# Performance work log

Measured on AMD Instinct MI355X. Metric: run time of the kernel, lower is better.

Reference implementation:

```python
import jax, jax.numpy as jnp
import numpy as np

BS = 1
H_ = 200
W_ = 200
NQ = H_ * W_          # 40000 BEV queries == num_value
D = 256
NH = 8
DH = D // NH          # 32
NL = 1
NP = 4
NQUEUE = 2
B2 = BS * NQUEUE


def setup_inputs() -> dict:
    key = jax.random.key(0)
    ks = jax.random.split(key, 12)
    s = 0.02
    inp = {
        "query": jax.random.normal(ks[0], (BS, NQ, D), jnp.float32),
        "query_pos": jax.random.normal(ks[1], (BS, NQ, D), jnp.float32) * 0.1,
        "reference_points": jax.random.uniform(ks[2], (BS, NQ, NL, 2), jnp.float32),
        # sampling_offsets linear: in = d_model*num_bev_queue, out = queue*heads*levels*points*2
        "W_so": jax.random.normal(ks[3], (D * NQUEUE, NQUEUE * NH * NL * NP * 2), jnp.float32) * s,
        "b_so": jax.random.normal(ks[4], (NQUEUE * NH * NL * NP * 2,), jnp.float32),
        # attention_weights linear: out = queue*heads*levels*points
        "W_aw": jax.random.normal(ks[5], (D * NQUEUE, NQUEUE * NH * NL * NP), jnp.float32) * s,
        "b_aw": jax.random.normal(ks[6], (NQUEUE * NH * NL * NP,), jnp.float32) * s,
        "W_v": jax.random.normal(ks[7], (D, D), jnp.float32) * s,
        "b_v": jax.random.normal(ks[8], (D,), jnp.float32) * s,
        "W_o": jax.random.normal(ks[9], (D, D), jnp.float32) * s,
        "b_o": jax.random.normal(ks[10], (D,), jnp.float32) * s,
    }
    return inp


def _deform_attn_single_level(v, loc, attn_w):
    """v: (B, Nv, NH, DH); loc: (B, Nq, NH, NP, 2) in [0,1]; attn_w: (B, Nq, NH, NP).
    grid_sample semantics: align_corners=False, zero padding."""
    B = v.shape[0]
    vt = v.transpose(0, 2, 1, 3)                      # (B, NH, Nv, DH)
    # pixel coords (align_corners=False): p = loc * size - 0.5
    x = (loc[..., 0] * W_ - 0.5).transpose(0, 2, 1, 3).reshape(B, NH, -1)  # (B, NH, Nq*NP)
    y = (loc[..., 1] * H_ - 0.5).transpose(0, 2, 1, 3).reshape(B, NH, -1)
    wt = attn_w.transpose(0, 2, 1, 3).reshape(B, NH, -1)
    x0f = jnp.floor(x); y0f = jnp.floor(y)
    x0 = x0f.astype(jnp.int32); y0 = y0f.astype(jnp.int32)
    x1 = x0 + 1; y1 = y0 + 1
    wx1 = x - x0f; wx0 = 1.0 - wx1
    wy1 = y - y0f; wy0 = 1.0 - wy1

    def corner(ix, iy, cw):
        valid = (ix >= 0) & (ix < W_) & (iy >= 0) & (iy < H_)
        idx = jnp.clip(iy, 0, H_ - 1) * W_ + jnp.clip(ix, 0, W_ - 1)
        g = jnp.take_along_axis(vt, idx[..., None], axis=2)   # (B, NH, Nq*NP, DH)
        return g * (cw * valid.astype(cw.dtype))[..., None]

    acc = (corner(x0, y0, wx0 * wy0) + corner(x1, y0, wx1 * wy0)
           + corner(x0, y1, wx0 * wy1) + corner(x1, y1, wx1 * wy1))
    acc = acc * wt[..., None]
    acc = acc.reshape(B, NH, -1, NP, DH).sum(3)               # (B, NH, Nq, DH)
    return acc.transpose(0, 2, 1, 3).reshape(B, -1, NH * DH)  # (B, Nq, D)


def reference(query, query_pos, reference_points, W_so, b_so, W_aw, b_aw, W_v, b_v, W_o, b_o):
    # input_flatten defaults to query (pre-positional); query gets pos added
    q = query + query_pos
    # default queue construction: duplicate current BEV -> (bs*queue, Nv, D)
    value = jnp.stack([query, query], axis=1).reshape(B2, NQ, D)
    history_bev = value[:BS]                                   # (bs, Nv, D)
    qwh = jnp.concatenate([history_bev, q], axis=-1)           # (bs, Nq, 2D)
    # value projection
    v = (value @ W_v + b_v).reshape(B2, NQ, NH, DH)
    # offsets / weights from concatenated features
    so = (qwh @ W_so + b_so).reshape(BS, NQ, NH, NQUEUE, NL, NP, 2)
    aw = (qwh @ W_aw + b_aw).reshape(BS, NQ, NH, NQUEUE, NL * NP)
    aw = jax.nn.softmax(aw, axis=-1).reshape(BS, NQ, NH, NQUEUE, NL, NP)
    aw = aw.transpose(0, 3, 1, 2, 4, 5).reshape(B2, NQ, NH, NL, NP)
    so = so.transpose(0, 3, 1, 2, 4, 5, 6).reshape(B2, NQ, NH, NL, NP, 2)
    # duplicate reference points across the queue
    rp = jnp.stack([reference_points] * NQUEUE, axis=1).reshape(B2, NQ, NL, 2)
    offset_norm = jnp.array([W_, H_], jnp.float32)             # (w, h)
    loc = rp[:, :, None, :, None, :] + so / offset_norm        # (B2, NQ, NH, NL, NP, 2)
    out = _deform_attn_single_level(v, loc[:, :, :, 0], aw[:, :, :, 0])  # (B2, NQ, D)
    # fuse queue outputs by mean (queue is the fast axis of B2)
    out = out.reshape(BS, NQUEUE, NQ, D).mean(axis=1)
    return out @ W_o + b_o
```

## Files before the change

kernel.cpp:

```cpp
#include <hip/hip_runtime.h>
#include <math.h>

#define NQc 40000
#define Wc 200
#define Hc 200

typedef __attribute__((ext_vector_type(8))) short short8;
typedef __attribute__((ext_vector_type(4))) float f32x4;
typedef __attribute__((ext_vector_type(2))) float f32x2;

#define VMWAIT(N) asm volatile("s_waitcnt vmcnt(" #N ")" ::: "memory")

__device__ __forceinline__ ushort f2b(float f) {
  unsigned u = __float_as_uint(f);
  u = (u + 0x7fffu + ((u >> 16) & 1u)) >> 16;
  return (ushort)u;
}

__device__ __forceinline__ void glds16(const void* g, void* l) {
  __builtin_amdgcn_global_load_lds(
      (const __attribute__((address_space(1))) void*)g,
      (__attribute__((address_space(3))) void*)l, 16, 0, 0);
}

__global__ __launch_bounds__(256) void prep_all(
    const float* __restrict__ q, const float* __restrict__ qp,
    const float* __restrict__ Wv, const float* __restrict__ Wo,
    const float* __restrict__ Wso, const float* __restrict__ Waw,
    ushort* __restrict__ qlo, ushort* __restrict__ qhi,
    ushort* __restrict__ WvT, ushort* __restrict__ WoT,
    ushort* __restrict__ WsoT, ushort* __restrict__ WawT) {
  const int bid = blockIdx.x;
  if (bid < 10000) {
    const int flat = bid * 256 + threadIdx.x;
    const int m = flat >> 6;
    const int c8 = (flat & 63) * 8;
    ushort o[8];
    if (c8 < 256) {
      const float4 a = *(const float4*)(q + (size_t)m * 256 + c8);
      const float4 b = *(const float4*)(q + (size_t)m * 256 + c8 + 4);
      o[0] = f2b(a.x); o[1] = f2b(a.y); o[2] = f2b(a.z); o[3] = f2b(a.w);
      o[4] = f2b(b.x); o[5] = f2b(b.y); o[6] = f2b(b.z); o[7] = f2b(b.w);
      *(uint4*)&qlo[(size_t)m * 256 + c8] = *(const uint4*)o;
    } else {
      const int c = c8 - 256;
      const float4 a  = *(const float4*)(q  + (size_t)m * 256 + c);
      const float4 b  = *(const float4*)(q  + (size_t)m * 256 + c + 4);
      const float4 ap = *(const float4*)(qp + (size_t)m * 256 + c);
      const float4 bp = *(const float4*)(qp + (size_t)m * 256 + c + 4);
      o[0] = f2b(a.x + ap.x); o[1] = f2b(a.y + ap.y);
      o[2] = f2b(a.z + ap.z); o[3] = f2b(a.w + ap.w);
      o[4] = f2b(b.x + bp.x); o[5] = f2b(b.y + bp.y);
      o[6] = f2b(b.z + bp.z); o[7] = f2b(b.w + bp.w);
      *(uint4*)&qhi[(size_t)m * 256 + c] = *(const uint4*)o;
    }
  } else {
    const int idx = (bid - 10000) * 256 + threadIdx.x;
    if (idx < 65536) {
      int n = idx >> 8, k = idx & 255;
      WvT[idx] = f2b(Wv[k * 256 + n]);
    } else if (idx < 131072) {
      int i = idx - 65536;
      int n = i >> 8, k = i & 255;
      WoT[i] = f2b(Wo[k * 256 + n]);
    } else if (idx < 196608) {
      int i = idx - 131072;
      int n = i >> 9, k = i & 511;
      WsoT[i] = f2b(Wso[k * 128 + n]);
    } else {
      int i = idx - 196608;
      int n = i >> 9, k = i & 511;
      WawT[i] = f2b(Waw[k * 64 + n]);
    }
  }
}


__global__ __launch_bounds__(256, 2) void gemm_soaw_k(
    const ushort* __restrict__ qlo, const ushort* __restrict__ qhi,
    const ushort* __restrict__ WsoT, const ushort* __restrict__ WawT,
    const float* __restrict__ b_so, const float* __restrict__ b_aw,
    float* __restrict__ so_ws, float* __restrict__ aw_ws) {
  __shared__ __align__(16) char smem[65536];
  float (*E)[68] = (float(*)[68])smem;
  f32x4 acc[12] = {};
  const int m0 = blockIdx.x * 64;
  const int tid = threadIdx.x;
  const int w = tid >> 6, lane = tid & 63;
  const int rl = lane & 15, q2 = lane >> 4;
  const int sw8 = rl & 7;
  const int lrow = lane >> 3, lch = (lane & 7) ^ (lrow & 7);

  auto STAGE = [&](int buf, int t) {
    ushort* As = (ushort*)(smem + buf * 32768);
    ushort* Bs = As + 4096;
    const int k0 = t * 64;
    const ushort* aq = (k0 < 256) ? qlo : qhi;
    const int ka = k0 & 255;
#pragma unroll
    for (int i = 0; i < 2; ++i) {
      const int g = w * 2 + i;
      const int row = g * 8 + lrow;
      glds16(aq + (size_t)(m0 + row) * 256 + ka + lch * 8,
             As + g * 512 + lane * 8);
    }
#pragma unroll
    for (int i = 0; i < 6; ++i) {
      const int g = w * 6 + i;
      const int row = g * 8 + lrow;
      const ushort* gsrc = (row < 128)
          ? WsoT + (size_t)row * 512 + k0 + lch * 8
          : WawT + (size_t)(row - 128) * 512 + k0 + lch * 8;
      glds16(gsrc, Bs + g * 512 + lane * 8);
    }
  };

  STAGE(0, 0);
#pragma unroll
  for (int t = 0; t < 8; ++t) {
    const int cur = t & 1;
    if (t < 7) {
      STAGE(cur ^ 1, t + 1);
      VMWAIT(8);
    } else {
      VMWAIT(0);
    }
    __builtin_amdgcn_s_barrier();
    {
      const ushort* Asb = (const ushort*)(smem + cur * 32768);
      const ushort* Bsb = Asb + 4096;
#pragma unroll
      for (int kk = 0; kk < 2; ++kk) {
        const short8 af = *(const short8*)
            &Asb[(w * 16 + rl) * 64 + ((kk * 4 + q2) ^ sw8) * 8];
#pragma unroll
        for (int nj = 0; nj < 12; ++nj) {
          const short8 bf = *(const short8*)
              &Bsb[(nj * 16 + rl) * 64 + ((kk * 4 + q2) ^ sw8) * 8];
          acc[nj] = __builtin_amdgcn_mfma_f32_16x16x32_bf16(af, bf, acc[nj], 0, 0, 0);
        }
      }
    }
    __builtin_amdgcn_s_barrier();
  }

  const int rbase = q2 * 4, cl = rl;
#pragma unroll
  for (int p = 0; p < 3; ++p) {
#pragma unroll
    for (int j = 0; j < 4; ++j) {
      const int nj = p * 4 + j;
      const int nl = j * 16 + cl;
      const f32x4 a = acc[nj];
      if (p < 2) {
        const float bb = b_so[p * 64 + nl];
#pragma unroll
        for (int r = 0; r < 4; ++r)
          E[w * 16 + rbase + r][nl] = a[r] + bb;
      } else {
        const float bb = b_aw[nl];
#pragma unroll
        for (int r = 0; r < 4; ++r) {
          float z = a[r] + bb;
          float zm = fmaxf(z, __shfl_xor(z, 1, 64));
          zm = fmaxf(zm, __shfl_xor(zm, 2, 64));
          float e = expf(z - zm);
          float s = e + __shfl_xor(e, 1, 64);
          s = s + __shfl_xor(s, 2, 64);
          E[w * 16 + rbase + r][nl] = e / s;
        }
      }
    }
    __syncthreads();
#pragma unroll
    for (int it = 0; it < 4; ++it) {
      const int flat = it * 256 + tid;
      const int row = flat >> 4, c4 = (flat & 15) * 4;
      const float4 vle = *(const float4*)&E[row][c4];
      if (p < 2)
        *(float4*)&so_ws[(size_t)(m0 + row) * 128 + p * 64 + c4] = vle;
      else
        *(float4*)&aw_ws[(size_t)(m0 + row) * 64 + c4] = vle;
    }
    __syncthreads();
  }
}

__global__ __launch_bounds__(256, 3) void gemm_v_k(
    const ushort* __restrict__ qlo, const ushort* __restrict__ WvT,
    const float* __restrict__ bv, ushort* __restrict__ vt) {
  __shared__ __align__(16) char smem[49152];
  ushort (*Eb)[72] = (ushort(*)[72])smem;
  f32x4 acc[8] = {};
  const int m0 = blockIdx.x * 64, n0 = blockIdx.y * 128;
  const int tid = threadIdx.x;
  const int w = tid >> 6, lane = tid & 63;
  const int rl = lane & 15, q2 = lane >> 4;
  const int sw8 = rl & 7;
  const int lrow = lane >> 3, lch = (lane & 7) ^ (lrow & 7);

  auto STAGE = [&](int buf, int t) {
    ushort* As = (ushort*)(smem + buf * 24576);
    ushort* Bs = As + 4096;
    const int k0 = t * 64;
#pragma unroll
    for (int i = 0; i < 2; ++i) {
      const int g = w * 2 + i;
      const int row = g * 8 + lrow;
      glds16(qlo + (size_t)(m0 + row) * 256 + k0 + lch * 8,
             As + g * 512 + lane * 8);
    }
#pragma unroll
    for (int i = 0; i < 4; ++i) {
      const int g = w * 4 + i;
      const int row = g * 8 + lrow;
      glds16(WvT + (size_t)(n0 + row) * 256 + k0 + lch * 8,
             Bs + g * 512 + lane * 8);
    }
  };

  STAGE(0, 0);
#pragma unroll
  for (int t = 0; t < 4; ++t) {
    const int cur = t & 1;
    if (t < 3) {
      STAGE(cur ^ 1, t + 1);
      VMWAIT(6);
    } else {
      VMWAIT(0);
    }
    __builtin_amdgcn_s_barrier();
    {
      const ushort* Asb = (const ushort*)(smem + cur * 24576);
      const ushort* Bsb = Asb + 4096;
#pragma unroll
      for (int kk = 0; kk < 2; ++kk) {
        const short8 af = *(const short8*)
            &Asb[(w * 16 + rl) * 64 + ((kk * 4 + q2) ^ sw8) * 8];
#pragma unroll
        for (int nj = 0; nj < 8; ++nj) {
          const short8 bf = *(const short8*)
              &Bsb[(nj * 16 + rl) * 64 + ((kk * 4 + q2) ^ sw8) * 8];
          acc[nj] = __builtin_amdgcn_mfma_f32_16x16x32_bf16(af, bf, acc[nj], 0, 0, 0);
        }
      }
    }
    __builtin_amdgcn_s_barrier();
  }

  const int rbase = q2 * 4, cl = rl;
#pragma unroll
  for (int p = 0; p < 2; ++p) {
#pragma unroll
    for (int j = 0; j < 4; ++j) {
      const int nj = p * 4 + j;
      const int n = n0 + p * 64 + j * 16 + cl;
      const float bb = bv[n];
      const f32x4 a = acc[nj];
#pragma unroll
      for (int r = 0; r < 4; ++r)
        Eb[w * 16 + rbase + r][j * 16 + cl] = f2b(a[r] + bb);
    }
    __syncthreads();
#pragma unroll
    for (int hh = 0; hh < 2; ++hh) {
      const int h = (n0 + p * 64) / 32 + hh;
#pragma unroll
      for (int it = 0; it < 2; ++it) {
        const int flat = it * 256 + tid;
        const int row = flat >> 3, d4 = (flat & 7) * 4;
        *(ushort4*)&vt[((size_t)h * NQc + m0 + row) * 32 + d4] =
            *(const ushort4*)&Eb[row][hh * 32 + d4];
      }
    }
    __syncthreads();
  }
}

__global__ __launch_bounds__(256, 3) void gemm_o_k(
    const ushort* __restrict__ Ap, const ushort* __restrict__ WoT,
    const float* __restrict__ bo, float* __restrict__ out) {
  __shared__ __align__(16) char smem[49152];
  float (*E)[68] = (float(*)[68])smem;
  f32x4 acc[8] = {};
  const int m0 = blockIdx.x * 64, n0 = blockIdx.y * 128;
  const int tid = threadIdx.x;
  const int w = tid >> 6, lane = tid & 63;
  const int rl = lane & 15, q2 = lane >> 4;
  const int sw8 = rl & 7;
  const int lrow = lane >> 3, lch = (lane & 7) ^ (lrow & 7);

  auto STAGE = [&](int buf, int t) {
    ushort* As = (ushort*)(smem + buf * 24576);
    ushort* Bs = As + 4096;
    const int k0 = t * 64;
#pragma unroll
    for (int i = 0; i < 2; ++i) {
      const int g = w * 2 + i;
      const int row = g * 8 + lrow;
      glds16(Ap + (size_t)(m0 + row) * 256 + k0 + lch * 8,
             As + g * 512 + lane * 8);
    }
#pragma unroll
    for (int i = 0; i < 4; ++i) {
      const int g = w * 4 + i;
      const int row = g * 8 + lrow;
      glds16(WoT + (size_t)(n0 + row) * 256 + k0 + lch * 8,
             Bs + g * 512 + lane * 8);
    }
  };

  STAGE(0, 0);
#pragma unroll
  for (int t = 0; t < 4; ++t) {
    const int cur = t & 1;
    if (t < 3) {
      STAGE(cur ^ 1, t + 1);
      VMWAIT(6);
    } else {
      VMWAIT(0);
    }
    __builtin_amdgcn_s_barrier();
    {
      const ushort* Asb = (const ushort*)(smem + cur * 24576);
      const ushort* Bsb = Asb + 4096;
#pragma unroll
      for (int kk = 0; kk < 2; ++kk) {
        const short8 af = *(const short8*)
            &Asb[(w * 16 + rl) * 64 + ((kk * 4 + q2) ^ sw8) * 8];
#pragma unroll
        for (int nj = 0; nj < 8; ++nj) {
          const short8 bf = *(const short8*)
              &Bsb[(nj * 16 + rl) * 64 + ((kk * 4 + q2) ^ sw8) * 8];
          acc[nj] = __builtin_amdgcn_mfma_f32_16x16x32_bf16(af, bf, acc[nj], 0, 0, 0);
        }
      }
    }
    __builtin_amdgcn_s_barrier();
  }

  const int rbase = q2 * 4, cl = rl;
#pragma unroll
  for (int p = 0; p < 2; ++p) {
#pragma unroll
    for (int j = 0; j < 4; ++j) {
      const int nj = p * 4 + j;
      const int n = n0 + p * 64 + j * 16 + cl;
      const float bb = bo[n];
      const f32x4 a = acc[nj];
#pragma unroll
      for (int r = 0; r < 4; ++r)
        E[w * 16 + rbase + r][j * 16 + cl] = a[r] + bb;
    }
    __syncthreads();
#pragma unroll
    for (int it = 0; it < 4; ++it) {
      const int flat = it * 256 + tid;
      const int row = flat >> 4, c4 = (flat & 15) * 4;
      *(float4*)&out[(size_t)(m0 + row) * 256 + n0 + p * 64 + c4] =
          *(const float4*)&E[row][c4];
    }
    __syncthreads();
  }
}

__global__ __launch_bounds__(256) void sample_kernel(
    const ushort* __restrict__ vt,
    const float* __restrict__ so_ws,
    const float* __restrict__ aw_ws,
    const float* __restrict__ refp,
    ushort* __restrict__ out_pre)
{
  __shared__ int2   offs[32][9];
  __shared__ float2 wts2[32][9][2];
  const int h  = blockIdx.x & 7;
  const int m0 = (blockIdx.x >> 3) * 32;
  const int tid = threadIdx.x;

  {
    const int j  = tid & 7;
    const int qi = tid >> 3;
    const int m  = m0 + qi;
    const int c  = h * 8 + j;
    const float sx  = so_ws[(size_t)m * 128 + c * 2 + 0];
    const float sy  = so_ws[(size_t)m * 128 + c * 2 + 1];
    const float wgt = 0.5f * aw_ws[(size_t)m * 64 + c];
    const float x = refp[m * 2 + 0] * (float)Wc + sx - 0.5f;
    const float y = refp[m * 2 + 1] * (float)Hc + sy - 0.5f;
    const float x0f = floorf(x), y0f = floorf(y);
    const int x0 = (int)x0f, y0 = (int)y0f;
    const int x1 = x0 + 1, y1 = y0 + 1;
    const float wx1 = x - x0f, wx0 = 1.0f - wx1;
    const float wy1 = y - y0f, wy0 = 1.0f - wy1;
    const float wx0v = (x0 >= 0 && x0 < Wc) ? wx0 : 0.0f;
    const float wx1v = (x1 >= 0 && x1 < Wc) ? wx1 : 0.0f;
    const float wy0v = ((y0 >= 0 && y0 < Hc) ? wy0 : 0.0f) * wgt;
    const float wy1v = ((y1 >= 0 && y1 < Hc) ? wy1 : 0.0f) * wgt;
    const int bx = min(max(x0, 0), Wc - 2);
    const float wl = (bx == x0) ? wx0v : ((bx == x1) ? wx1v : 0.0f);
    const float wr = (bx + 1 == x1) ? wx1v : ((bx + 1 == x0) ? wx0v : 0.0f);
    const int cy0 = min(max(y0, 0), Hc - 1);
    const int cy1 = min(max(y1, 0), Hc - 1);
    offs[qi][j] = make_int2((cy0 * Wc + bx) * 64, (cy1 * Wc + bx) * 64);
    wts2[qi][j][0] = make_float2(wl * wy0v, wl * wy1v);
    wts2[qi][j][1] = make_float2(wr * wy0v, wr * wy1v);
  }
  __syncthreads();

  const int qi = tid >> 3;
  const int ld = tid & 7;
  const int m  = m0 + qi;
  const int hf = ld >> 2;
  const char* __restrict__ vb =
      (const char*)(vt + (size_t)h * NQc * 32) + (uint)(ld * 16);

  uint4 raw[16];
#pragma unroll
  for (int j = 0; j < 8; ++j) {
    const int2 oo = offs[qi][j];
    raw[2 * j]     = *(const uint4*)(vb + (uint)oo.x);
    raw[2 * j + 1] = *(const uint4*)(vb + (uint)oo.y);
  }
  __builtin_amdgcn_sched_barrier(0);

  f32x2 acc0 = {0.0f, 0.0f}, acc1 = {0.0f, 0.0f};
  f32x2 acc2 = {0.0f, 0.0f}, acc3 = {0.0f, 0.0f};

#pragma unroll
  for (int j = 0; j < 8; ++j) {
    const float2 wp = wts2[qi][j][hf];
#pragma unroll
    for (int r = 0; r < 2; ++r) {
      const uint4 rawv = raw[2 * j + r];
      const float w = (r == 0) ? wp.x : wp.y;
      const f32x2 wv = {w, w};
      f32x2 v0, v1, v2, v3;
      v0.x = __uint_as_float(rawv.x << 16);
      v0.y = __uint_as_float(rawv.x & 0xFFFF0000u);
      v1.x = __uint_as_float(rawv.y << 16);
      v1.y = __uint_as_float(rawv.y & 0xFFFF0000u);
      v2.x = __uint_as_float(rawv.z << 16);
      v2.y = __uint_as_float(rawv.z & 0xFFFF0000u);
      v3.x = __uint_as_float(rawv.w << 16);
      v3.y = __uint_as_float(rawv.w & 0xFFFF0000u);
#if __has_builtin(__builtin_elementwise_fma)
      acc0 = __builtin_elementwise_fma(wv, v0, acc0);
      acc1 = __builtin_elementwise_fma(wv, v1, acc1);
      acc2 = __builtin_elementwise_fma(wv, v2, acc2);
      acc3 = __builtin_elementwise_fma(wv, v3, acc3);
#else
      acc0.x = fmaf(w, v0.x, acc0.x); acc0.y = fmaf(w, v0.y, acc0.y);
      acc1.x = fmaf(w, v1.x, acc1.x); acc1.y = fmaf(w, v1.y, acc1.y);
      acc2.x = fmaf(w, v2.x, acc2.x); acc2.y = fmaf(w, v2.y, acc2.y);
      acc3.x = fmaf(w, v3.x, acc3.x); acc3.y = fmaf(w, v3.y, acc3.y);
#endif
    }
  }

  float a[8] = {acc0.x, acc0.y, acc1.x, acc1.y,
                acc2.x, acc2.y, acc3.x, acc3.y};
#pragma unroll
  for (int k = 0; k < 8; ++k) a[k] += __shfl_xor(a[k], 4, 64);

  if (hf == 0) {
    ushort rr[8];
#pragma unroll
    for (int k = 0; k < 8; ++k) rr[k] = f2b(a[k]);
    *(uint4*)&out_pre[(size_t)m * 256 + h * 32 + ld * 8] = *(const uint4*)rr;
  }
}

extern "C" void kernel_launch(void* const* d_in, const int* in_sizes, int n_in,
                              void* d_out, int out_size, void* d_ws, size_t ws_size,
                              hipStream_t stream) {
  const float* query     = (const float*)d_in[0];
  const float* query_pos = (const float*)d_in[1];
  const float* refp      = (const float*)d_in[2];
  const float* W_so      = (const float*)d_in[3];
  const float* b_so      = (const float*)d_in[4];
  const float* W_aw      = (const float*)d_in[5];
  const float* b_aw      = (const float*)d_in[6];
  const float* W_v       = (const float*)d_in[7];
  const float* b_v       = (const float*)d_in[8];
  const float* W_o       = (const float*)d_in[9];
  const float* b_o       = (const float*)d_in[10];
  float* out = (float*)d_out;

  char* base = (char*)d_ws;
  ushort* qlo     = (ushort*)base;
  ushort* qhi     = (ushort*)(base + 20480000);
  ushort* vt      = (ushort*)(base + 20480000);
  ushort* out_pre = (ushort*)base;
  float*  so_ws   = (float*)(base + 40960000);
  float*  aw_ws   = (float*)(base + 61440000);
  ushort* WvT     = (ushort*)(base + 71680000);
  ushort* WoT     = WvT + 65536;
  ushort* WsoT    = WoT + 65536;
  ushort* WawT    = WsoT + 65536;

  prep_all<<<10896, 256, 0, stream>>>(query, query_pos, W_v, W_o, W_so, W_aw,
                                      qlo, qhi, WvT, WoT, WsoT, WawT);
  gemm_soaw_k<<<625, 256, 0, stream>>>(qlo, qhi, WsoT, WawT,
                                       b_so, b_aw, so_ws, aw_ws);
  gemm_v_k<<<dim3(625, 2), 256, 0, stream>>>(qlo, WvT, b_v, vt);
  sample_kernel<<<10000, 256, 0, stream>>>(vt, so_ws, aw_ws, refp, out_pre);
  gemm_o_k<<<dim3(625, 2), 256, 0, stream>>>(out_pre, WoT, b_o, out);
}
```

Baseline: 226.6 us.

## Fuse query bf16 conversion, value GEMM and offset/weight GEMM into one kernel

The query and query_pos conversion to bf16 now happens directly into shared memory inside a single fused front kernel. That kernel computes both the value projection and the sampling-offset/attention-weight projection from the same resident A tile, so the qlo/qhi intermediates are no longer written to and read back from global memory, and two launches are removed. In exchange it uses 128KB of LDS and large accumulator register sets, which limits occupancy to one block per CU with only 625 blocks.

Measured after the change: 237.6 us. 4.9% more time.

```diff
diff --git a/kernel.cpp b/kernel.cpp
--- a/kernel.cpp
+++ b/kernel.cpp
@@ -23,67 +23,44 @@
       (__attribute__((address_space(3))) void*)l, 16, 0, 0);
 }
 
-__global__ __launch_bounds__(256) void prep_all(
-    const float* __restrict__ q, const float* __restrict__ qp,
+__global__ __launch_bounds__(256) void prep_w(
     const float* __restrict__ Wv, const float* __restrict__ Wo,
     const float* __restrict__ Wso, const float* __restrict__ Waw,
-    ushort* __restrict__ qlo, ushort* __restrict__ qhi,
     ushort* __restrict__ WvT, ushort* __restrict__ WoT,
     ushort* __restrict__ WsoT, ushort* __restrict__ WawT) {
-  const int bid = blockIdx.x;
-  if (bid < 10000) {
-    const int flat = bid * 256 + threadIdx.x;
-    const int m = flat >> 6;
-    const int c8 = (flat & 63) * 8;
-    ushort o[8];
-    if (c8 < 256) {
-      const float4 a = *(const float4*)(q + (size_t)m * 256 + c8);
-      const float4 b = *(const float4*)(q + (size_t)m * 256 + c8 + 4);
-      o[0] = f2b(a.x); o[1] = f2b(a.y); o[2] = f2b(a.z); o[3] = f2b(a.w);
-      o[4] = f2b(b.x); o[5] = f2b(b.y); o[6] = f2b(b.z); o[7] = f2b(b.w);
-      *(uint4*)&qlo[(size_t)m * 256 + c8] = *(const uint4*)o;
-    } else {
-      const int c = c8 - 256;
-      const float4 a  = *(const float4*)(q  + (size_t)m * 256 + c);
-      const float4 b  = *(const float4*)(q  + (size_t)m * 256 + c + 4);
-      const float4 ap = *(const float4*)(qp + (size_t)m * 256 + c);
-      const float4 bp = *(const float4*)(qp + (size_t)m * 256 + c + 4);
-      o[0] = f2b(a.x + ap.x); o[1] = f2b(a.y + ap.y);
-      o[2] = f2b(a.z + ap.z); o[3] = f2b(a.w + ap.w);
-      o[4] = f2b(b.x + bp.x); o[5] = f2b(b.y + bp.y);
-      o[6] = f2b(b.z + bp.z); o[7] = f2b(b.w + bp.w);
-      *(uint4*)&qhi[(size_t)m * 256 + c] = *(const uint4*)o;
-    }
+  const int idx = blockIdx.x * 256 + threadIdx.x;
+  if (idx < 65536) {
+    int n = idx >> 8, k = idx & 255;
+    WvT[idx] = f2b(Wv[k * 256 + n]);
+  } else if (idx < 131072) {
+    int i = idx - 65536;
+    int n = i >> 8, k = i & 255;
+    WoT[i] = f2b(Wo[k * 256 + n]);
+  } else if (idx < 196608) {
+    int i = idx - 131072;
+    int n = i >> 9, k = i & 511;
+    WsoT[i] = f2b(Wso[k * 128 + n]);
   } else {
-    const int idx = (bid - 10000) * 256 + threadIdx.x;
-    if (idx < 65536) {
-      int n = idx >> 8, k = idx & 255;
-      WvT[idx] = f2b(Wv[k * 256 + n]);
-    } else if (idx < 131072) {
-      int i = idx - 65536;
-      int n = i >> 8, k = i & 255;
-      WoT[i] = f2b(Wo[k * 256 + n]);
-    } else if (idx < 196608) {
-      int i = idx - 131072;
-      int n = i >> 9, k = i & 511;
-      WsoT[i] = f2b(Wso[k * 128 + n]);
-    } else {
-      int i = idx - 196608;
-      int n = i >> 9, k = i & 511;
-      WawT[i] = f2b(Waw[k * 64 + n]);
-    }
-  }
-}
-
-
-__global__ __launch_bounds__(256, 2) void gemm_soaw_k(
-    const ushort* __restrict__ qlo, const ushort* __restrict__ qhi,
-    const ushort* __restrict__ WsoT, const ushort* __restrict__ WawT,
-    const float* __restrict__ b_so, const float* __restrict__ b_aw,
-    float* __restrict__ so_ws, float* __restrict__ aw_ws) {
-  __shared__ __align__(16) char smem[65536];
-  float (*E)[68] = (float(*)[68])smem;
-  f32x4 acc[12] = {};
+    int i = idx - 196608;
+    int n = i >> 9, k = i & 511;
+    WawT[i] = f2b(Waw[k * 64 + n]);
+  }
+}
+
+__global__ __launch_bounds__(256, 1) void fused_front(
+    const float* __restrict__ q, const float* __restrict__ qp,
+    const ushort* __restrict__ WvT, const ushort* __restrict__ WsoT,
+    const ushort* __restrict__ WawT,
+    const float* __restrict__ bv, const float* __restrict__ b_so,
+    const float* __restrict__ b_aw,
+    ushort* __restrict__ vt, float* __restrict__ so_ws,
+    float* __restrict__ aw_ws) {
+  __shared__ __align__(16) char smem[131072];
+  ushort* Ab = (ushort*)smem;
+  float (*E)[68] = (float(*)[68])(smem + 65536);
+  ushort (*Eb)[72] = (ushort(*)[72])(smem + 65536);
+  f32x4 vacc[16] = {};
+  f32x4 sacc[12] = {};
   const int m0 = blockIdx.x * 64;
   const int tid = threadIdx.x;
   const int w = tid >> 6, lane = tid & 63;
@@ -91,53 +68,94 @@
   const int sw8 = rl & 7;
   const int lrow = lane >> 3, lch = (lane & 7) ^ (lrow & 7);
 
-  auto STAGE = [&](int buf, int t) {
-    ushort* As = (ushort*)(smem + buf * 32768);
-    ushort* Bs = As + 4096;
+  {
+    const int arow = tid >> 2, qn = tid & 3;
+    const float* qr  = q  + (size_t)(m0 + arow) * 256 + qn * 64;
+    const float* qpr = qp + (size_t)(m0 + arow) * 256 + qn * 64;
+    ushort* Alo = Ab + arow * 256;
+    ushort* Ahi = Ab + 16384 + arow * 256;
+    const int swz = arow & 7;
+#pragma unroll
+    for (int i = 0; i < 4; ++i) {
+      float4 a[4], p[4];
+#pragma unroll
+      for (int k = 0; k < 4; ++k) a[k] = *(const float4*)(qr + i * 16 + k * 4);
+#pragma unroll
+      for (int k = 0; k < 4; ++k) p[k] = *(const float4*)(qpr + i * 16 + k * 4);
+      ushort lo[16], hi[16];
+#pragma unroll
+      for (int k = 0; k < 4; ++k) {
+        lo[k * 4 + 0] = f2b(a[k].x); lo[k * 4 + 1] = f2b(a[k].y);
+        lo[k * 4 + 2] = f2b(a[k].z); lo[k * 4 + 3] = f2b(a[k].w);
+        hi[k * 4 + 0] = f2b(a[k].x + p[k].x); hi[k * 4 + 1] = f2b(a[k].y + p[k].y);
+        hi[k * 4 + 2] = f2b(a[k].z + p[k].z); hi[k * 4 + 3] = f2b(a[k].w + p[k].w);
+      }
+      const int cb = qn * 8 + i * 2;
+      *(uint4*)&Alo[(cb ^ swz) * 8]       = *(const uint4*)&lo[0];
+      *(uint4*)&Alo[((cb + 1) ^ swz) * 8] = *(const uint4*)&lo[8];
+      *(uint4*)&Ahi[(cb ^ swz) * 8]       = *(const uint4*)&hi[0];
+      *(uint4*)&Ahi[((cb + 1) ^ swz) * 8] = *(const uint4*)&hi[8];
+    }
+  }
+  __syncthreads();
+
+  auto STAGEV = [&](int buf, int t) {
+    ushort* Bs = (ushort*)(smem + 65536 + buf * 32768);
     const int k0 = t * 64;
-    const ushort* aq = (k0 < 256) ? qlo : qhi;
-    const int ka = k0 & 255;
-#pragma unroll
-    for (int i = 0; i < 2; ++i) {
-      const int g = w * 2 + i;
+#pragma unroll
+    for (int i = 0; i < 8; ++i) {
+      const int g = w * 8 + i;
       const int row = g * 8 + lrow;
-      glds16(aq + (size_t)(m0 + row) * 256 + ka + lch * 8,
-             As + g * 512 + lane * 8);
-    }
+      glds16(WvT + (size_t)row * 256 + k0 + lch * 8, Bs + g * 512 + lane * 8);
+    }
+  };
+  auto STAGES = [&](int buf, int s) {
+    ushort* Bs = (ushort*)(smem + 65536 + buf * 32768);
+    const int k0 = s * 64;
 #pragma unroll
     for (int i = 0; i < 6; ++i) {
       const int g = w * 6 + i;
       const int row = g * 8 + lrow;
-      const ushort* gsrc = (row < 128)
+      const ushort* src = (row < 128)
           ? WsoT + (size_t)row * 512 + k0 + lch * 8
           : WawT + (size_t)(row - 128) * 512 + k0 + lch * 8;
-      glds16(gsrc, Bs + g * 512 + lane * 8);
+      glds16(src, Bs + g * 512 + lane * 8);
     }
   };
 
-  STAGE(0, 0);
-#pragma unroll
-  for (int t = 0; t < 8; ++t) {
-    const int cur = t & 1;
-    if (t < 7) {
-      STAGE(cur ^ 1, t + 1);
-      VMWAIT(8);
-    } else {
-      VMWAIT(0);
-    }
+  STAGEV(0, 0);
+#pragma unroll
+  for (int u = 0; u < 12; ++u) {
+    if (u < 3)        { STAGEV((u + 1) & 1, u + 1); VMWAIT(8); }
+    else if (u == 3)  { STAGES(0, 0);               VMWAIT(6); }
+    else if (u < 11)  { STAGES((u + 1) & 1, u - 3); VMWAIT(6); }
+    else              { VMWAIT(0); }
     __builtin_amdgcn_s_barrier();
-    {
-      const ushort* Asb = (const ushort*)(smem + cur * 32768);
-      const ushort* Bsb = Asb + 4096;
+    const ushort* Bs = (const ushort*)(smem + 65536 + (u & 1) * 32768);
+    if (u < 4) {
 #pragma unroll
       for (int kk = 0; kk < 2; ++kk) {
         const short8 af = *(const short8*)
-            &Asb[(w * 16 + rl) * 64 + ((kk * 4 + q2) ^ sw8) * 8];
+            &Ab[(w * 16 + rl) * 256 + ((u * 8 + kk * 4 + q2) ^ sw8) * 8];
+#pragma unroll
+        for (int nj = 0; nj < 16; ++nj) {
+          const short8 bf = *(const short8*)
+              &Bs[(nj * 16 + rl) * 64 + ((kk * 4 + q2) ^ sw8) * 8];
+          vacc[nj] = __builtin_amdgcn_mfma_f32_16x16x32_bf16(af, bf, vacc[nj], 0, 0, 0);
+        }
+      }
+    } else {
+      const int s = u - 4, sel = s >> 2, tl = s & 3;
+#pragma unroll
+      for (int kk = 0; kk < 2; ++kk) {
+        const short8 af = *(const short8*)
+            &Ab[sel * 16384 + (w * 16 + rl) * 256 +
+                ((tl * 8 + kk * 4 + q2) ^ sw8) * 8];
 #pragma unroll
         for (int nj = 0; nj < 12; ++nj) {
           const short8 bf = *(const short8*)
-              &Bsb[(nj * 16 + rl) * 64 + ((kk * 4 + q2) ^ sw8) * 8];
-          acc[nj] = __builtin_amdgcn_mfma_f32_16x16x32_bf16(af, bf, acc[nj], 0, 0, 0);
+              &Bs[(nj * 16 + rl) * 64 + ((kk * 4 + q2) ^ sw8) * 8];
+          sacc[nj] = __builtin_amdgcn_mfma_f32_16x16x32_bf16(af, bf, sacc[nj], 0, 0, 0);
         }
       }
     }
@@ -145,13 +163,41 @@
   }
 
   const int rbase = q2 * 4, cl = rl;
+
+#pragma unroll
+  for (int p4 = 0; p4 < 4; ++p4) {
+#pragma unroll
+    for (int j = 0; j < 4; ++j) {
+      const int nj = p4 * 4 + j;
+      const int n = p4 * 64 + j * 16 + cl;
+      const float bb = bv[n];
+      const f32x4 a = vacc[nj];
+#pragma unroll
+      for (int r = 0; r < 4; ++r)
+        Eb[w * 16 + rbase + r][j * 16 + cl] = f2b(a[r] + bb);
+    }
+    __syncthreads();
+#pragma unroll
+    for (int hh = 0; hh < 2; ++hh) {
+      const int h = p4 * 2 + hh;
+#pragma unroll
+      for (int it = 0; it < 2; ++it) {
+        const int flat = it * 256 + tid;
+        const int row = flat >> 3, d4 = (flat & 7) * 4;
+        *(ushort4*)&vt[((size_t)h * NQc + m0 + row) * 32 + d4] =
+            *(const ushort4*)&Eb[row][hh * 32 + d4];
+      }
+    }
+    __syncthreads();
+  }
+
 #pragma unroll
   for (int p = 0; p < 3; ++p) {
 #pragma unroll
     for (int j = 0; j < 4; ++j) {
       const int nj = p * 4 + j;
       const int nl = j * 16 + cl;
-      const f32x4 a = acc[nj];
+      const f32x4 a = sacc[nj];
       if (p < 2) {
         const float bb = b_so[p * 64 + nl];
 #pragma unroll
@@ -181,97 +227,6 @@
         *(float4*)&so_ws[(size_t)(m0 + row) * 128 + p * 64 + c4] = vle;
       else
         *(float4*)&aw_ws[(size_t)(m0 + row) * 64 + c4] = vle;
-    }
-    __syncthreads();
-  }
-}
-
-__global__ __launch_bounds__(256, 3) void gemm_v_k(
-    const ushort* __restrict__ qlo, const ushort* __restrict__ WvT,
-    const float* __restrict__ bv, ushort* __restrict__ vt) {
-  __shared__ __align__(16) char smem[49152];
-  ushort (*Eb)[72] = (ushort(*)[72])smem;
-  f32x4 acc[8] = {};
-  const int m0 = blockIdx.x * 64, n0 = blockIdx.y * 128;
-  const int tid = threadIdx.x;
-  const int w = tid >> 6, lane = tid & 63;
-  const int rl = lane & 15, q2 = lane >> 4;
-  const int sw8 = rl & 7;
-  const int lrow = lane >> 3, lch = (lane & 7) ^ (lrow & 7);
-
-  auto STAGE = [&](int buf, int t) {
-    ushort* As = (ushort*)(smem + buf * 24576);
-    ushort* Bs = As + 4096;
-    const int k0 = t * 64;
-#pragma unroll
-    for (int i = 0; i < 2; ++i) {
-      const int g = w * 2 + i;
-      const int row = g * 8 + lrow;
-      glds16(qlo + (size_t)(m0 + row) * 256 + k0 + lch * 8,
-             As + g * 512 + lane * 8);
-    }
-#pragma unroll
-    for (int i = 0; i < 4; ++i) {
-      const int g = w * 4 + i;
-      const int row = g * 8 + lrow;
-      glds16(WvT + (size_t)(n0 + row) * 256 + k0 + lch * 8,
-             Bs + g * 512 + lane * 8);
-    }
-  };
-
-  STAGE(0, 0);
-#pragma unroll
-  for (int t = 0; t < 4; ++t) {
-    const int cur = t & 1;
-    if (t < 3) {
-      STAGE(cur ^ 1, t + 1);
-      VMWAIT(6);
-    } else {
-      VMWAIT(0);
-    }
-    __builtin_amdgcn_s_barrier();
-    {
-      const ushort* Asb = (const ushort*)(smem + cur * 24576);
-      const ushort* Bsb = Asb + 4096;
-#pragma unroll
-      for (int kk = 0; kk < 2; ++kk) {
-        const short8 af = *(const short8*)
-            &Asb[(w * 16 + rl) * 64 + ((kk * 4 + q2) ^ sw8) * 8];
-#pragma unroll
-        for (int nj = 0; nj < 8; ++nj) {
-          const short8 bf = *(const short8*)
-              &Bsb[(nj * 16 + rl) * 64 + ((kk * 4 + q2) ^ sw8) * 8];
-          acc[nj] = __builtin_amdgcn_mfma_f32_16x16x32_bf16(af, bf, acc[nj], 0, 0, 0);
-        }
-      }
-    }
-    __builtin_amdgcn_s_barrier();
-  }
-
-  const int rbase = q2 * 4, cl = rl;
-#pragma unroll
-  for (int p = 0; p < 2; ++p) {
-#pragma unroll
-    for (int j = 0; j < 4; ++j) {
-      const int nj = p * 4 + j;
-      const int n = n0 + p * 64 + j * 16 + cl;
-      const float bb = bv[n];
-      const f32x4 a = acc[nj];
-#pragma unroll
-      for (int r = 0; r < 4; ++r)
-        Eb[w * 16 + rbase + r][j * 16 + cl] = f2b(a[r] + bb);
-    }
-    __syncthreads();
-#pragma unroll
-    for (int hh = 0; hh < 2; ++hh) {
-      const int h = (n0 + p * 64) / 32 + hh;
-#pragma unroll
-      for (int it = 0; it < 2; ++it) {
-        const int flat = it * 256 + tid;
-        const int row = flat >> 3, d4 = (flat & 7) * 4;
-        *(ushort4*)&vt[((size_t)h * NQc + m0 + row) * 32 + d4] =
-            *(const ushort4*)&Eb[row][hh * 32 + d4];
-      }
     }
     __syncthreads();
   }
@@ -487,22 +442,18 @@
   float* out = (float*)d_out;
 
   char* base = (char*)d_ws;
-  ushort* qlo     = (ushort*)base;
-  ushort* qhi     = (ushort*)(base + 20480000);
-  ushort* vt      = (ushort*)(base + 20480000);
-  ushort* out_pre = (ushort*)base;
-  float*  so_ws   = (float*)(base + 40960000);
-  float*  aw_ws   = (float*)(base + 61440000);
+  ushort* vt      = (ushort*)base;
+  float*  so_ws   = (float*)(base + 20480000);
+  float*  aw_ws   = (float*)(base + 40960000);
+  ushort* out_pre = (ushort*)(base + 51200000);
   ushort* WvT     = (ushort*)(base + 71680000);
   ushort* WoT     = WvT + 65536;
   ushort* WsoT    = WoT + 65536;
   ushort* WawT    = WsoT + 65536;
 
-  prep_all<<<10896, 256, 0, stream>>>(query, query_pos, W_v, W_o, W_so, W_aw,
-                                      qlo, qhi, WvT, WoT, WsoT, WawT);
-  gemm_soaw_k<<<625, 256, 0, stream>>>(qlo, qhi, WsoT, WawT,
-                                       b_so, b_aw, so_ws, aw_ws);
-  gemm_v_k<<<dim3(625, 2), 256, 0, stream>>>(qlo, WvT, b_v, vt);
+  prep_w<<<896, 256, 0, stream>>>(W_v, W_o, W_so, W_aw, WvT, WoT, WsoT, WawT);
+  fused_front<<<625, 256, 0, stream>>>(query, query_pos, WvT, WsoT, WawT,
+                                       b_v, b_so, b_aw, vt, so_ws, aw_ws);
   sample_kernel<<<10000, 256, 0, stream>>>(vt, so_ws, aw_ws, refp, out_pre);
   gemm_o_k<<<dim3(625, 2), 256, 0, stream>>>(out_pre, WoT, b_o, out);
 }
```

## Merge value and offset/weight GEMMs into one launch; fuse q conversion reads

Applied to the files above, without the earlier changes.

The prep kernel now has each thread read query and query_pos once and write both the bf16 query and bf16 query+pos rows, so query is no longer loaded twice. When the workspace is large enough, the value-projection GEMM and the sampling-offset/attention-weight GEMM run as one heterogeneous launch with block ranges split by blockIdx. That needs a separate vt buffer so vt no longer aliases qhi. The merge removes a kernel launch and lets both GEMMs fill the GPU together, at the cost of a larger workspace and mixed block shapes with different shared-memory footprints in the same grid.

Result: no change. 226.0 us, median of 3 (-0.3%).

```diff
diff --git a/kernel.cpp b/kernel.cpp
--- a/kernel.cpp
+++ b/kernel.cpp
@@ -31,31 +31,25 @@
     ushort* __restrict__ WvT, ushort* __restrict__ WoT,
     ushort* __restrict__ WsoT, ushort* __restrict__ WawT) {
   const int bid = blockIdx.x;
-  if (bid < 10000) {
+  if (bid < 5000) {
     const int flat = bid * 256 + threadIdx.x;
-    const int m = flat >> 6;
-    const int c8 = (flat & 63) * 8;
-    ushort o[8];
-    if (c8 < 256) {
-      const float4 a = *(const float4*)(q + (size_t)m * 256 + c8);
-      const float4 b = *(const float4*)(q + (size_t)m * 256 + c8 + 4);
-      o[0] = f2b(a.x); o[1] = f2b(a.y); o[2] = f2b(a.z); o[3] = f2b(a.w);
-      o[4] = f2b(b.x); o[5] = f2b(b.y); o[6] = f2b(b.z); o[7] = f2b(b.w);
-      *(uint4*)&qlo[(size_t)m * 256 + c8] = *(const uint4*)o;
-    } else {
-      const int c = c8 - 256;
-      const float4 a  = *(const float4*)(q  + (size_t)m * 256 + c);
-      const float4 b  = *(const float4*)(q  + (size_t)m * 256 + c + 4);
-      const float4 ap = *(const float4*)(qp + (size_t)m * 256 + c);
-      const float4 bp = *(const float4*)(qp + (size_t)m * 256 + c + 4);
-      o[0] = f2b(a.x + ap.x); o[1] = f2b(a.y + ap.y);
-      o[2] = f2b(a.z + ap.z); o[3] = f2b(a.w + ap.w);
-      o[4] = f2b(b.x + bp.x); o[5] = f2b(b.y + bp.y);
-      o[6] = f2b(b.z + bp.z); o[7] = f2b(b.w + bp.w);
-      *(uint4*)&qhi[(size_t)m * 256 + c] = *(const uint4*)o;
-    }
+    const int m = flat >> 5;
+    const int c8 = (flat & 31) * 8;
+    const float4 a  = *(const float4*)(q  + (size_t)m * 256 + c8);
+    const float4 b  = *(const float4*)(q  + (size_t)m * 256 + c8 + 4);
+    const float4 ap = *(const float4*)(qp + (size_t)m * 256 + c8);
+    const float4 bp = *(const float4*)(qp + (size_t)m * 256 + c8 + 4);
+    ushort lo[8], hi[8];
+    lo[0] = f2b(a.x); lo[1] = f2b(a.y); lo[2] = f2b(a.z); lo[3] = f2b(a.w);
+    lo[4] = f2b(b.x); lo[5] = f2b(b.y); lo[6] = f2b(b.z); lo[7] = f2b(b.w);
+    hi[0] = f2b(a.x + ap.x); hi[1] = f2b(a.y + ap.y);
+    hi[2] = f2b(a.z + ap.z); hi[3] = f2b(a.w + ap.w);
+    hi[4] = f2b(b.x + bp.x); hi[5] = f2b(b.y + bp.y);
+    hi[6] = f2b(b.z + bp.z); hi[7] = f2b(b.w + bp.w);
+    *(uint4*)&qlo[(size_t)m * 256 + c8] = *(const uint4*)lo;
+    *(uint4*)&qhi[(size_t)m * 256 + c8] = *(const uint4*)hi;
   } else {
-    const int idx = (bid - 10000) * 256 + threadIdx.x;
+    const int idx = (bid - 5000) * 256 + threadIdx.x;
     if (idx < 65536) {
       int n = idx >> 8, k = idx & 255;
       WvT[idx] = f2b(Wv[k * 256 + n]);
@@ -119,12 +113,8 @@
 #pragma unroll
   for (int t = 0; t < 8; ++t) {
     const int cur = t & 1;
-    if (t < 7) {
-      STAGE(cur ^ 1, t + 1);
-      VMWAIT(8);
-    } else {
-      VMWAIT(0);
-    }
+    if (t < 7) { STAGE(cur ^ 1, t + 1); VMWAIT(8); }
+    else       { VMWAIT(0); }
     __builtin_amdgcn_s_barrier();
     {
       const ushort* Asb = (const ushort*)(smem + cur * 32768);
@@ -223,12 +213,8 @@
 #pragma unroll
   for (int t = 0; t < 4; ++t) {
     const int cur = t & 1;
-    if (t < 3) {
-      STAGE(cur ^ 1, t + 1);
-      VMWAIT(6);
-    } else {
-      VMWAIT(0);
-    }
+    if (t < 3) { STAGE(cur ^ 1, t + 1); VMWAIT(6); }
+    else       { VMWAIT(0); }
     __builtin_amdgcn_s_barrier();
     {
       const ushort* Asb = (const ushort*)(smem + cur * 24576);
@@ -274,6 +260,196 @@
       }
     }
     __syncthreads();
+  }
+}
+
+__global__ __launch_bounds__(256, 2) void gemm_front(
+    const ushort* __restrict__ qlo, const ushort* __restrict__ qhi,
+    const ushort* __restrict__ WvT, const ushort* __restrict__ WsoT,
+    const ushort* __restrict__ WawT,
+    const float* __restrict__ bv, const float* __restrict__ b_so,
+    const float* __restrict__ b_aw,
+    ushort* __restrict__ vt, float* __restrict__ so_ws,
+    float* __restrict__ aw_ws) {
+  __shared__ __align__(16) char smem[65536];
+  const int tid = threadIdx.x;
+  const int w = tid >> 6, lane = tid & 63;
+  const int rl = lane & 15, q2 = lane >> 4;
+  const int sw8 = rl & 7;
+  const int lrow = lane >> 3, lch = (lane & 7) ^ (lrow & 7);
+  const int bid = blockIdx.x;
+
+  if (bid < 1250) {
+    ushort (*Eb)[72] = (ushort(*)[72])smem;
+    f32x4 acc[8] = {};
+    const int m0 = (bid >> 1) * 64, n0 = (bid & 1) * 128;
+
+    auto STAGE = [&](int buf, int t) {
+      ushort* As = (ushort*)(smem + buf * 24576);
+      ushort* Bs = As + 4096;
+      const int k0 = t * 64;
+#pragma unroll
+      for (int i = 0; i < 2; ++i) {
+        const int g = w * 2 + i;
+        const int row = g * 8 + lrow;
+        glds16(qlo + (size_t)(m0 + row) * 256 + k0 + lch * 8,
+               As + g * 512 + lane * 8);
+      }
+#pragma unroll
+      for (int i = 0; i < 4; ++i) {
+        const int g = w * 4 + i;
+        const int row = g * 8 + lrow;
+        glds16(WvT + (size_t)(n0 + row) * 256 + k0 + lch * 8,
+               Bs + g * 512 + lane * 8);
+      }
+    };
+
+    STAGE(0, 0);
+#pragma unroll
+    for (int t = 0; t < 4; ++t) {
+      const int cur = t & 1;
+      if (t < 3) { STAGE(cur ^ 1, t + 1); VMWAIT(6); }
+      else       { VMWAIT(0); }
+      __builtin_amdgcn_s_barrier();
+      {
+        const ushort* Asb = (const ushort*)(smem + cur * 24576);
+        const ushort* Bsb = Asb + 4096;
+#pragma unroll
+        for (int kk = 0; kk < 2; ++kk) {
+          const short8 af = *(const short8*)
+              &Asb[(w * 16 + rl) * 64 + ((kk * 4 + q2) ^ sw8) * 8];
+#pragma unroll
+          for (int nj = 0; nj < 8; ++nj) {
+            const short8 bf = *(const short8*)
+                &Bsb[(nj * 16 + rl) * 64 + ((kk * 4 + q2) ^ sw8) * 8];
+            acc[nj] = __builtin_amdgcn_mfma_f32_16x16x32_bf16(af, bf, acc[nj], 0, 0, 0);
+          }
+        }
+      }
+      __builtin_amdgcn_s_barrier();
+    }
+
+    const int rbase = q2 * 4, cl = rl;
+#pragma unroll
+    for (int p = 0; p < 2; ++p) {
+#pragma unroll
+      for (int j = 0; j < 4; ++j) {
+        const int nj = p * 4 + j;
+        const int n = n0 + p * 64 + j * 16 + cl;
+        const float bb = bv[n];
+        const f32x4 a = acc[nj];
+#pragma unroll
+        for (int r = 0; r < 4; ++r)
+          Eb[w * 16 + rbase + r][j * 16 + cl] = f2b(a[r] + bb);
+      }
+      __syncthreads();
+#pragma unroll
+      for (int hh = 0; hh < 2; ++hh) {
+        const int h = (n0 + p * 64) / 32 + hh;
+#pragma unroll
+        for (int it = 0; it < 2; ++it) {
+          const int flat = it * 256 + tid;
+          const int row = flat >> 3, d4 = (flat & 7) * 4;
+          *(ushort4*)&vt[((size_t)h * NQc + m0 + row) * 32 + d4] =
+              *(const ushort4*)&Eb[row][hh * 32 + d4];
+        }
+      }
+      __syncthreads();
+    }
+  } else {
+    float (*E)[68] = (float(*)[68])smem;
+    f32x4 acc[12] = {};
+    const int m0 = (bid - 1250) * 64;
+
+    auto STAGE = [&](int buf, int t) {
+      ushort* As = (ushort*)(smem + buf * 32768);
+      ushort* Bs = As + 4096;
+      const int k0 = t * 64;
+      const ushort* aq = (k0 < 256) ? qlo : qhi;
+      const int ka = k0 & 255;
+#pragma unroll
+      for (int i = 0; i < 2; ++i) {
+        const int g = w * 2 + i;
+        const int row = g * 8 + lrow;
+        glds16(aq + (size_t)(m0 + row) * 256 + ka + lch * 8,
+               As + g * 512 + lane * 8);
+      }
+#pragma unroll
+      for (int i = 0; i < 6; ++i) {
+        const int g = w * 6 + i;
+        const int row = g * 8 + lrow;
+        const ushort* gsrc = (row < 128)
+            ? WsoT + (size_t)row * 512 + k0 + lch * 8
+            : WawT + (size_t)(row - 128) * 512 + k0 + lch * 8;
+        glds16(gsrc, Bs + g * 512 + lane * 8);
+      }
+    };
+
+    STAGE(0, 0);
+#pragma unroll
+    for (int t = 0; t < 8; ++t) {
+      const int cur = t & 1;
+      if (t < 7) { STAGE(cur ^ 1, t + 1); VMWAIT(8); }
+      else       { VMWAIT(0); }
+      __builtin_amdgcn_s_barrier();
+      {
+        const ushort* Asb = (const ushort*)(smem + cur * 32768);
+        const ushort* Bsb = Asb + 4096;
+#pragma unroll
+        for (int kk = 0; kk < 2; ++kk) {
+          const short8 af = *(const short8*)
+              &Asb[(w * 16 + rl) * 64 + ((kk * 4 + q2) ^ sw8) * 8];
+#pragma unroll
+          for (int nj = 0; nj < 12; ++nj) {
+            const short8 bf = *(const short8*)
+                &Bsb[(nj * 16 + rl) * 64 + ((kk * 4 + q2) ^ sw8) * 8];
+            acc[nj] = __builtin_amdgcn_mfma_f32_16x16x32_bf16(af, bf, acc[nj], 0, 0, 0);
+          }
+        }
+      }
+      __builtin_amdgcn_s_barrier();
+    }
+
+    const int rbase = q2 * 4, cl = rl;
+#pragma unroll
+    for (int p = 0; p < 3; ++p) {
+#pragma unroll
+      for (int j = 0; j < 4; ++j) {
+        const int nj = p * 4 + j;
+        const int nl = j * 16 + cl;
+        const f32x4 a = acc[nj];
+        if (p < 2) {
+          const float bb = b_so[p * 64 + nl];
+#pragma unroll
+          for (int r = 0; r < 4; ++r)
+            E[w * 16 + rbase + r][nl] = a[r] + bb;
+        } else {
+          const float bb = b_aw[nl];
+#pragma unroll
+          for (int r = 0; r < 4; ++r) {
+            float z = a[r] + bb;
+            float zm = fmaxf(z, __shfl_xor(z, 1, 64));
+            zm = fmaxf(zm, __shfl_xor(zm, 2, 64));
+            float e = expf(z - zm);
+            float s = e + __shfl_xor(e, 1, 64);
+            s = s + __shfl_xor(s, 2, 64);
+            E[w * 16 + rbase + r][nl] = e / s;
+          }
+        }
+      }
+      __syncthreads();
+#pragma unroll
+      for (int it = 0; it < 4; ++it) {
+        const int flat = it * 256 + tid;
+        const int row = flat >> 4, c4 = (flat & 15) * 4;
+        const float4 vle = *(const float4*)&E[row][c4];
+        if (p < 2)
+          *(float4*)&so_ws[(size_t)(m0 + row) * 128 + p * 64 + c4] = vle;
+        else
+          *(float4*)&aw_ws[(size_t)(m0 + row) * 64 + c4] = vle;
+      }
+      __syncthreads();
+    }
   }
 }
 
@@ -314,12 +490,8 @@
 #pragma unroll
   for (int t = 0; t < 4; ++t) {
     const int cur = t & 1;
-    if (t < 3) {
-      STAGE(cur ^ 1, t + 1);
-      VMWAIT(6);
-    } else {
-      VMWAIT(0);
-    }
+    if (t < 3) { STAGE(cur ^ 1, t + 1); VMWAIT(6); }
+    else       { VMWAIT(0); }
     __builtin_amdgcn_s_barrier();
     {
       const ushort* Asb = (const ushort*)(smem + cur * 24576);
@@ -485,24 +657,44 @@
   const float* W_o       = (const float*)d_in[9];
   const float* b_o       = (const float*)d_in[10];
   float* out = (float*)d_out;
-
   char* base = (char*)d_ws;
-  ushort* qlo     = (ushort*)base;
-  ushort* qhi     = (ushort*)(base + 20480000);
-  ushort* vt      = (ushort*)(base + 20480000);
-  ushort* out_pre = (ushort*)base;
-  float*  so_ws   = (float*)(base + 40960000);
-  float*  aw_ws   = (float*)(base + 61440000);
-  ushort* WvT     = (ushort*)(base + 71680000);
-  ushort* WoT     = WvT + 65536;
-  ushort* WsoT    = WoT + 65536;
-  ushort* WawT    = WsoT + 65536;
-
-  prep_all<<<10896, 256, 0, stream>>>(query, query_pos, W_v, W_o, W_so, W_aw,
-                                      qlo, qhi, WvT, WoT, WsoT, WawT);
-  gemm_soaw_k<<<625, 256, 0, stream>>>(qlo, qhi, WsoT, WawT,
-                                       b_so, b_aw, so_ws, aw_ws);
-  gemm_v_k<<<dim3(625, 2), 256, 0, stream>>>(qlo, WvT, b_v, vt);
-  sample_kernel<<<10000, 256, 0, stream>>>(vt, so_ws, aw_ws, refp, out_pre);
-  gemm_o_k<<<dim3(625, 2), 256, 0, stream>>>(out_pre, WoT, b_o, out);
-}
+
+  if (ws_size >= (size_t)92618752) {
+    ushort* qlo     = (ushort*)base;
+    ushort* qhi     = (ushort*)(base + 20480000);
+    ushort* vt      = (ushort*)(base + 40960000);
+    float*  so_ws   = (float*)(base + 61440000);
+    float*  aw_ws   = (float*)(base + 81920000);
+    ushort* out_pre = (ushort*)base;
+    ushort* WvT     = (ushort*)(base + 92160000);
+    ushort* WoT     = WvT + 65536;
+    ushort* WsoT    = WoT + 65536;
+    ushort* WawT    = WsoT + 65536;
+
+    prep_all<<<5896, 256, 0, stream>>>(query, query_pos, W_v, W_o, W_so, W_aw,
+                                       qlo, qhi, WvT, WoT, WsoT, WawT);
+    gemm_front<<<1875, 256, 0, stream>>>(qlo, qhi, WvT, WsoT, WawT,
+                                         b_v, b_so, b_aw, vt, so_ws, aw_ws);
+    sample_kernel<<<10000, 256, 0, stream>>>(vt, so_ws, aw_ws, refp, out_pre);
+    gemm_o_k<<<dim3(625, 2), 256, 0, stream>>>(out_pre, WoT, b_o, out);
+  } else {
+    ushort* qlo     = (ushort*)base;
+    ushort* qhi     = (ushort*)(base + 20480000);
+    ushort* vt      = (ushort*)(base + 20480000);
+    ushort* out_pre = (ushort*)base;
+    float*  so_ws   = (float*)(base + 40960000);
+    float*  aw_ws   = (float*)(base + 61440000);
+    ushort* WvT     = (ushort*)(base + 71680000);
+    ushort* WoT     = WvT + 65536;
+    ushort* WsoT    = WoT + 65536;
+    ushort* WawT    = WsoT + 65536;
+
+    prep_all<<<5896, 256, 0, stream>>>(query, query_pos, W_v, W_o, W_so, W_aw,
+                                       qlo, qhi, WvT, WoT, WsoT, WawT);
+    gemm_soaw_k<<<625, 256, 0, stream>>>(qlo, qhi, WsoT, WawT,
+                                         b_so, b_aw, so_ws, aw_ws);
+    gemm_v_k<<<dim3(625, 2), 256, 0, stream>>>(qlo, WvT, b_v, vt);
+    sample_kernel<<<10000, 256, 0, stream>>>(vt, so_ws, aw_ws, refp, out_pre);
+    gemm_o_k<<<dim3(625, 2), 256, 0, stream>>>(out_pre, WoT, b_o, out);
+  }
+}
```
